# Kernel tuning notes

Hardware: AMD Instinct MI355X
Metric: run time of the kernel (lower is better)

Reference implementation:

```python
import jax, jax.numpy as jnp
import numpy as np

N_NODES = 10000
N_EDGES = 320000
FIN = 2
HID = 64
OUT = 16
B = 4
T = 12


def _gcn_norm(src, dst, w, n):
    # add self loops (fill value 1.0, improved=False), then symmetric normalization
    loop = jnp.arange(n, dtype=src.dtype)
    src = jnp.concatenate([src, loop])
    dst = jnp.concatenate([dst, loop])
    w = jnp.concatenate([w, jnp.ones((n,), w.dtype)])
    deg = jax.ops.segment_sum(w, dst, num_segments=n)
    dinv = jnp.where(deg > 0, 1.0 / jnp.sqrt(deg), 0.0)
    return src, dst, dinv[src] * w * dinv[dst]


def _gcn_conv(x_nbf, src, dst, norm, W, b, n):
    # x_nbf: [N,B,F] ; GCNConv: (x W) aggregated with normalized weights, + bias
    xw = jnp.einsum('nbf,fh->nbh', x_nbf, W)          # [N,B,H]
    msgs = xw[src] * norm[:, None, None]               # [E',B,H]
    return jax.ops.segment_sum(msgs, dst, num_segments=n) + b


def setup_inputs() -> dict:
    key = jax.random.key(0)
    ks = jax.random.split(key, 20)
    x = jax.random.normal(ks[0], (B, N_NODES, FIN, T), jnp.float32)
    edge_index = jax.random.randint(ks[1], (2, N_EDGES), 0, N_NODES, jnp.int64 if jax.config.jax_enable_x64 else jnp.int32)
    edge_weight = jax.random.uniform(ks[2], (N_EDGES,), jnp.float32)
    s = 0.1
    p = {
        'Wz': s * jax.random.normal(ks[3], (FIN, HID), jnp.float32),
        'bz': jnp.zeros((HID,), jnp.float32),
        'Wr': s * jax.random.normal(ks[4], (FIN, HID), jnp.float32),
        'br': jnp.zeros((HID,), jnp.float32),
        'Wh': s * jax.random.normal(ks[5], (FIN, HID), jnp.float32),
        'bh': jnp.zeros((HID,), jnp.float32),
        'Lz_w': s * jax.random.normal(ks[6], (2 * HID, HID), jnp.float32),
        'Lz_b': jnp.zeros((HID,), jnp.float32),
        'Lr_w': s * jax.random.normal(ks[7], (2 * HID, HID), jnp.float32),
        'Lr_b': jnp.zeros((HID,), jnp.float32),
        'Lh_w': s * jax.random.normal(ks[8], (2 * HID, HID), jnp.float32),
        'Lh_b': jnp.zeros((HID,), jnp.float32),
        'lin_w': s * jax.random.normal(ks[9], (HID, OUT), jnp.float32),
        'lin_b': jnp.zeros((OUT,), jnp.float32),
    }
    return dict(x=x, edge_index=edge_index, edge_weight=edge_weight, **p)


def reference(x, edge_index, edge_weight, Wz, bz, Wr, br, Wh, bh,
              Lz_w, Lz_b, Lr_w, Lr_b, Lh_w, Lh_b, lin_w, lin_b):
    Bd, N, Fin, Td = x.shape
    src, dst, norm = _gcn_norm(edge_index[0], edge_index[1], edge_weight, N)
    H0 = jnp.zeros((N, Bd, Wz.shape[1]), x.dtype)
    xs = jnp.transpose(x, (3, 1, 0, 2))  # [T,N,B,Fin]

    def step(H, xt):
        cz = _gcn_conv(xt, src, dst, norm, Wz, bz, N)
        Z = jax.nn.sigmoid(jnp.concatenate([cz, H], -1) @ Lz_w + Lz_b)
        cr = _gcn_conv(xt, src, dst, norm, Wr, br, N)
        R = jax.nn.sigmoid(jnp.concatenate([cr, H], -1) @ Lr_w + Lr_b)
        ch = _gcn_conv(xt, src, dst, norm, Wh, bh, N)
        H_tilde = jnp.tanh(jnp.concatenate([ch, H * R], -1) @ Lh_w + Lh_b)
        Hn = Z * H + (1.0 - Z) * H_tilde
        out_t = jax.nn.relu(Hn) @ lin_w + lin_b  # [N,B,OUT]
        return Hn, out_t

    _, outs = jax.lax.scan(step, H0, xs)        # [T,N,B,OUT]
    return jnp.transpose(outs, (2, 0, 1, 3))     # [B,T,N,OUT]
```

## Files before the change

### kernel.cpp

```cpp
#include <hip/hip_runtime.h>
#include <cstdint>
#include <cstddef>

#define NN      10000
#define NE      320000
#define FINF    2
#define HIDN    64
#define OUTN    16
#define BBATCH  4
#define TSTEPS  12
#define NBROWS  (NN * BBATCH)
#define XTN     (TSTEPS * NN * BBATCH * FINF)
#define CAP     96

typedef _Float16 v8h __attribute__((ext_vector_type(8)));
typedef _Float16 v2h __attribute__((ext_vector_type(2)));
typedef float    v4f __attribute__((ext_vector_type(4)));

extern "C" __global__ void setup_kernel(const float* __restrict__ x,
                             const int* __restrict__ src, const int* __restrict__ dst,
                             const float* __restrict__ ew,
                             int* __restrict__ cnt, float* __restrict__ degf,
                             int2* __restrict__ bucket, _Float16* __restrict__ xAll,
                             const float* __restrict__ Wz, const float* __restrict__ bz,
                             const float* __restrict__ Wr, const float* __restrict__ br,
                             const float* __restrict__ Wh, const float* __restrict__ bh,
                             const float* __restrict__ Lz, const float* __restrict__ Lz_b,
                             const float* __restrict__ Lr, const float* __restrict__ Lr_b,
                             const float* __restrict__ Lh, const float* __restrict__ Lh_b,
                             const float* __restrict__ linw, const float* __restrict__ linb,
                             float* __restrict__ PP) {
    int idx = blockIdx.x * 256 + threadIdx.x;
    if (idx < NN) {
        const int n = idx;
        v8h* xo = (v8h*)(xAll + (size_t)n * 96);
        v8h vv[TSTEPS];
        #pragma unroll
        for (int b = 0; b < BBATCH; ++b) {
            const v4f* xp4 = (const v4f*)(x + ((size_t)b * NN + n) * 24);
            v4f c0 = xp4[0], c1 = xp4[1], c2 = xp4[2];
            v4f c3 = xp4[3], c4 = xp4[4], c5 = xp4[5];
            float f0[TSTEPS] = {c0.x, c0.y, c0.z, c0.w, c1.x, c1.y, c1.z, c1.w,
                                c2.x, c2.y, c2.z, c2.w};
            float f1[TSTEPS] = {c3.x, c3.y, c3.z, c3.w, c4.x, c4.y, c4.z, c4.w,
                                c5.x, c5.y, c5.z, c5.w};
            #pragma unroll
            for (int t = 0; t < TSTEPS; ++t) {
                vv[t][b * 2]     = (_Float16)f0[t];
                vv[t][b * 2 + 1] = (_Float16)f1[t];
            }
        }
        #pragma unroll
        for (int t = 0; t < TSTEPS; ++t) xo[t] = vv[t];
    }
    if (idx < NE) {
        int d = dst[idx];
        int s = src[idx];
        float w = ew[idx];
        int p = atomicAdd(&cnt[d], 1);
        if (p < CAP) {
            int2 rec;
            rec.x = s;
            rec.y = __float_as_int(w);
            bucket[d * CAP + p] = rec;
        }
        atomicAdd(&degf[d], w);
    }
    if (idx < 13904) {
        const float* Lg[3]    = {Lz, Lr, Lh};
        const float* Lbias[3] = {Lz_b, Lr_b, Lh_b};
        const float* Wg[3]    = {Wz, Wr, Wh};
        const float* bg[3]    = {bz, br, bh};
        int i = idx;
        if (i < 12288) {
            int g = i >> 12, rr = (i >> 6) & 63, j = i & 63;
            PP[i] = Lg[g][(64 + rr) * 64 + j];
        } else if (i < 12672) {
            int i2 = i - 12288;
            int g = i2 >> 7, f = (i2 >> 6) & 1, j = i2 & 63;
            float s = 0.f;
            for (int k = 0; k < 64; ++k) s = fmaf(Wg[g][f * 64 + k], Lg[g][k * 64 + j], s);
            PP[i] = s;
        } else if (i < 12864) {
            int i3 = i - 12672;
            int g = i3 >> 6, j = i3 & 63;
            float s = Lbias[g][j];
            for (int k = 0; k < 64; ++k) s = fmaf(bg[g][k], Lg[g][k * 64 + j], s);
            PP[i] = s;
        } else if (i < 13888) {
            PP[i] = linw[i - 12864];
        } else {
            PP[i] = linb[i - 13888];
        }
    }
}

__device__ __forceinline__ float fsigmoid(float x) {
    return __builtin_amdgcn_rcpf(1.0f + __builtin_amdgcn_exp2f(-1.442695041f * x));
}

extern "C" __global__ __launch_bounds__(256, 3)
void fused_kernel(const _Float16* __restrict__ xAll, const int2* __restrict__ bucket,
                  const int* __restrict__ cnt, const float* __restrict__ degf,
                  const float* __restrict__ PP, float* __restrict__ out) {
    __shared__ _Float16 WTH[64 * 72 + 32];
    __shared__ _Float16 WIZR[2 * 64 * 8 + 32];
    __shared__ _Float16 Hm[4][16 * 72];
    __shared__ float    aggL[16 * 96];
    __shared__ int      s_src[16 * CAP];
    __shared__ float    s_c[16 * CAP];
    __shared__ int      s_cnt[16];
    const int tid = threadIdx.x;
    const int w   = tid >> 6;
    const int l   = tid & 63;
    const int m   = l & 15;
    const int q   = l >> 4;
    const int n0  = blockIdx.x * 16 + w * 4 + q;

    {
        const int nl = tid >> 4;
        const int u  = tid & 15;
        const int ng = blockIdx.x * 16 + nl;
        const int c  = min(cnt[ng], CAP);
        if (u == 0) s_cnt[nl] = c;
        const float dn = rsqrtf(1.0f + degf[ng]);
        for (int i = u; i < c; i += 16) {
            int2 rec = bucket[ng * CAP + i];
            int s = rec.x;
            s_src[nl * CAP + i] = s;
            s_c[nl * CAP + i]   = __int_as_float(rec.y) * dn * rsqrtf(1.0f + degf[s]);
        }
    }

    for (int i = tid; i < 4096; i += 256) {
        int k = i >> 6, n = i & 63;
        WTH[n * 72 + k] = (_Float16)PP[8192 + i];
    }
    for (int i = tid; i < 64 * 8; i += 256) {
        int n = i >> 3, kk = i & 7;
        float v = 0.f;
        if (kk == 0)      v = PP[12288 + 2 * 128 + n];
        else if (kk == 1) v = PP[12288 + 2 * 128 + 64 + n];
        else if (kk == 2) v = PP[12672 + 2 * 64 + n];
        WTH[n * 72 + 64 + kk] = (_Float16)v;
    }
    for (int i = tid; i < 32; i += 256) WTH[64 * 72 + i] = (_Float16)0.f;
    for (int i = tid; i < 2 * 64 * 8; i += 256) {
        int g = i >> 9, rem = i & 511, n = rem >> 3, kk = rem & 7;
        float v = 0.f;
        if (kk == 0)      v = PP[12288 + g * 128 + n];
        else if (kk == 1) v = PP[12288 + g * 128 + 64 + n];
        else if (kk == 2) v = PP[12672 + g * 64 + n];
        WIZR[(g * 64 + n) * 8 + kk] = (_Float16)v;
    }
    for (int i = tid; i < 32; i += 256) WIZR[1024 + i] = (_Float16)0.f;

    __syncthreads();

    {
        const int nl = tid >> 4;
        const int u  = tid & 15;
        const int ng = blockIdx.x * 16 + nl;
        const int c  = s_cnt[nl];
        const float dn = rsqrtf(1.0f + degf[ng]);
        const v2h* x2 = (const v2h*)xAll;
        float acc[6];
        {
            v2h a = x2[(size_t)ng * 48 + u * 3];
            v2h b = x2[(size_t)ng * 48 + u * 3 + 1];
            v2h e = x2[(size_t)ng * 48 + u * 3 + 2];
            float c0 = dn * dn;
            acc[0] = c0 * (float)a.x; acc[1] = c0 * (float)a.y;
            acc[2] = c0 * (float)b.x; acc[3] = c0 * (float)b.y;
            acc[4] = c0 * (float)e.x; acc[5] = c0 * (float)e.y;
        }
        for (int i = 0; i < c; ++i) {
            int s    = s_src[nl * CAP + i];
            float cc = s_c[nl * CAP + i];
            v2h a = x2[(size_t)s * 48 + u * 3];
            v2h b = x2[(size_t)s * 48 + u * 3 + 1];
            v2h e = x2[(size_t)s * 48 + u * 3 + 2];
            acc[0] = fmaf(cc, (float)a.x, acc[0]);
            acc[1] = fmaf(cc, (float)a.y, acc[1]);
            acc[2] = fmaf(cc, (float)b.x, acc[2]);
            acc[3] = fmaf(cc, (float)b.y, acc[3]);
            acc[4] = fmaf(cc, (float)e.x, acc[4]);
            acc[5] = fmaf(cc, (float)e.y, acc[5]);
        }
        #pragma unroll
        for (int jj = 0; jj < 6; ++jj) aggL[nl * 96 + u * 6 + jj] = acc[jj];
    }

    v8h BZ[4][2], BR[4][2];
    #pragma unroll
    for (int nt = 0; nt < 4; ++nt) {
        #pragma unroll
        for (int c = 0; c < 2; ++c) {
            #pragma unroll
            for (int i = 0; i < 8; ++i) {
                int k = c * 32 + q * 8 + i;
                BZ[nt][c][i] = (_Float16)PP[k * 64 + nt * 16 + m];
                BR[nt][c][i] = (_Float16)PP[4096 + k * 64 + nt * 16 + m];
            }
        }
    }
    v8h linB0, linB1;
    #pragma unroll
    for (int i = 0; i < 8; ++i) {
        linB0[i] = (_Float16)PP[12864 + (q * 8 + i) * 16 + m];
        linB1[i] = (_Float16)PP[12864 + (32 + q * 8 + i) * 16 + m];
    }
    const float linbv = PP[13888 + m];

    __syncthreads();

    _Float16* __restrict__ Hw = &Hm[w][0];
    const int wsw = (q & 2) << 3;
    const _Float16* __restrict__ Ard = Hw + m * 72 + ((q ^ ((m >> 2) & 2)) * 8);
    const int aggBase = (w * 4 + (m >> 2)) * 96 + (m & 3) * 2;

    float Hold[4][4];
    #pragma unroll
    for (int nt = 0; nt < 4; ++nt)
        #pragma unroll
        for (int r = 0; r < 4; ++r) Hold[nt][r] = 0.f;
    v8h aH0{}, aH1{};

    const v4f zeroc = {0.f, 0.f, 0.f, 0.f};
    float* __restrict__ op = out + (size_t)n0 * 16 + m;

    for (int t = 0; t < TSTEPS; ++t) {
        v8h aI{};
        if (q == 0) {
            const float2 av = *(const float2*)&aggL[aggBase + t * 8];
            aI[0] = (_Float16)av.x;
            aI[1] = (_Float16)av.y;
            aI[2] = (_Float16)1.0f;
        }

        v4f accZ[4], accR[4];
        #pragma unroll
        for (int nt = 0; nt < 4; ++nt) {
            const v8h bIz = *(const v8h*)&WIZR[(0 * 64 + nt * 16 + m) * 8 + q * 8];
            const v8h bIr = *(const v8h*)&WIZR[(1 * 64 + nt * 16 + m) * 8 + q * 8];
            accZ[nt] = __builtin_amdgcn_mfma_f32_16x16x32_f16(aI,  bIz,       zeroc,    0, 0, 0);
            accZ[nt] = __builtin_amdgcn_mfma_f32_16x16x32_f16(aH0, BZ[nt][0], accZ[nt], 0, 0, 0);
            accZ[nt] = __builtin_amdgcn_mfma_f32_16x16x32_f16(aH1, BZ[nt][1], accZ[nt], 0, 0, 0);
            accR[nt] = __builtin_amdgcn_mfma_f32_16x16x32_f16(aI,  bIr,       zeroc,    0, 0, 0);
            accR[nt] = __builtin_amdgcn_mfma_f32_16x16x32_f16(aH0, BR[nt][0], accR[nt], 0, 0, 0);
            accR[nt] = __builtin_amdgcn_mfma_f32_16x16x32_f16(aH1, BR[nt][1], accR[nt], 0, 0, 0);
        }

        float Z[4][4];
        #pragma unroll
        for (int nt = 0; nt < 4; ++nt) {
            #pragma unroll
            for (int r = 0; r < 4; ++r) {
                Z[nt][r] = fsigmoid(accZ[nt][r]);
                float hr = Hold[nt][r] * fsigmoid(accR[nt][r]);
                Hw[(q * 4 + r) * 72 + ((nt * 16 + m) ^ wsw)] = (_Float16)hr;
            }
        }
        __threadfence_block();
        const v8h aP0 = *(const v8h*)Ard;
        const v8h aP1 = *(const v8h*)(Ard + 32);

        v4f accH[4];
        #pragma unroll
        for (int nt = 0; nt < 4; ++nt) {
            const _Float16* bh = &WTH[(nt * 16 + m) * 72 + q * 8];
            accH[nt] = __builtin_amdgcn_mfma_f32_16x16x32_f16(aI,  *(const v8h*)(bh + 64), zeroc,    0, 0, 0);
            accH[nt] = __builtin_amdgcn_mfma_f32_16x16x32_f16(aP0, *(const v8h*)bh,        accH[nt], 0, 0, 0);
            accH[nt] = __builtin_amdgcn_mfma_f32_16x16x32_f16(aP1, *(const v8h*)(bh + 32), accH[nt], 0, 0, 0);
        }

        #pragma unroll
        for (int nt = 0; nt < 4; ++nt) {
            #pragma unroll
            for (int r = 0; r < 4; ++r) {
                float ht = fmaf(2.0f, fsigmoid(2.0f * accH[nt][r]), -1.0f);
                float hn = Z[nt][r] * Hold[nt][r] + (1.f - Z[nt][r]) * ht;
                Hold[nt][r] = hn;
                Hw[(q * 4 + r) * 72 + ((nt * 16 + m) ^ wsw)] = (_Float16)hn;
            }
        }
        __threadfence_block();
        aH0 = *(const v8h*)Ard;
        aH1 = *(const v8h*)(Ard + 32);

        const v8h zz{};
        v8h r0 = __builtin_elementwise_max(aH0, zz);
        v8h r1 = __builtin_elementwise_max(aH1, zz);
        v4f accO = {linbv, linbv, linbv, linbv};
        accO = __builtin_amdgcn_mfma_f32_16x16x32_f16(r0, linB0, accO, 0, 0, 0);
        accO = __builtin_amdgcn_mfma_f32_16x16x32_f16(r1, linB1, accO, 0, 0, 0);
        #pragma unroll
        for (int r = 0; r < 4; ++r)
            op[(size_t)r * (TSTEPS * NN * 16)] = accO[r];
        op += NN * 16;
    }
}


extern "C" void kernel_launch(void* const* d_in, const int* in_sizes, int n_in,
                              void* d_out, int out_size, void* d_ws, size_t ws_size,
                              hipStream_t stream) {
    const float* x   = (const float*)d_in[0];
    const int*   ei  = (const int*)d_in[1];
    const float* ew  = (const float*)d_in[2];
    const float* Wz  = (const float*)d_in[3];
    const float* bz  = (const float*)d_in[4];
    const float* Wr  = (const float*)d_in[5];
    const float* br  = (const float*)d_in[6];
    const float* Wh  = (const float*)d_in[7];
    const float* bh  = (const float*)d_in[8];
    const float* Lz  = (const float*)d_in[9];
    const float* Lz_b= (const float*)d_in[10];
    const float* Lr  = (const float*)d_in[11];
    const float* Lr_b= (const float*)d_in[12];
    const float* Lh  = (const float*)d_in[13];
    const float* Lh_b= (const float*)d_in[14];
    const float* lw  = (const float*)d_in[15];
    const float* lb  = (const float*)d_in[16];
    float* out = (float*)d_out;

    char* ws = (char*)d_ws;
    size_t off = 0;
    auto alloc = [&](size_t bytes) -> char* {
        char* p = ws + off;
        off += (bytes + 15) & ~(size_t)15;
        return p;
    };
    _Float16* xAll = (_Float16*)alloc((size_t)XTN * 2);
    float* PP      = (float*)alloc(13904 * 4);
    int2*  bucket  = (int2*) alloc((size_t)NN * CAP * 8);
    int*   cnt     = (int*)  alloc(NN * 4);
    float* degf    = (float*)alloc(NN * 4);

    const int* srcp = ei;
    const int* dstp = ei + NE;

    hipMemsetAsync(cnt, 0, 2 * NN * sizeof(int), stream);
    setup_kernel<<<(NE + 255) / 256, 256, 0, stream>>>(x, srcp, dstp, ew, cnt, degf,
                                                       bucket, xAll,
                                                       Wz, bz, Wr, br, Wh, bh,
                                                       Lz, Lz_b, Lr, Lr_b, Lh, Lh_b,
                                                       lw, lb, PP);
    fused_kernel<<<NN / 16, 256, 0, stream>>>(xAll, bucket, cnt, degf, PP, out);
}
```

Measured before the change: 193.8 us.

## Merge setup and fused kernels into one persistent kernel with grid barrier

Combines the bucketing/setup kernel and the main recurrent kernel into a single launch, with a global atomic-counter grid barrier between the two phases, which removes one kernel launch and the gap between them. Edge processing becomes a grid-stride loop over 625 blocks. The design depends on all 625 blocks being co-resident (3 blocks per CU is requested on 256 CUs), otherwise the barrier deadlocks. Spinning on the barrier and the smaller grid used for the edge phase can also add latency.

```diff
diff --git a/kernel.cpp b/kernel.cpp
--- a/kernel.cpp
+++ b/kernel.cpp
@@ -12,27 +12,46 @@
 #define NBROWS  (NN * BBATCH)
 #define XTN     (TSTEPS * NN * BBATCH * FINF)
 #define CAP     96
+#define NBLK    (NN / 16)
+#define GT      (NBLK * 256)
 
 typedef _Float16 v8h __attribute__((ext_vector_type(8)));
 typedef _Float16 v2h __attribute__((ext_vector_type(2)));
 typedef float    v4f __attribute__((ext_vector_type(4)));
 
-extern "C" __global__ void setup_kernel(const float* __restrict__ x,
-                             const int* __restrict__ src, const int* __restrict__ dst,
-                             const float* __restrict__ ew,
-                             int* __restrict__ cnt, float* __restrict__ degf,
-                             int2* __restrict__ bucket, _Float16* __restrict__ xAll,
-                             const float* __restrict__ Wz, const float* __restrict__ bz,
-                             const float* __restrict__ Wr, const float* __restrict__ br,
-                             const float* __restrict__ Wh, const float* __restrict__ bh,
-                             const float* __restrict__ Lz, const float* __restrict__ Lz_b,
-                             const float* __restrict__ Lr, const float* __restrict__ Lr_b,
-                             const float* __restrict__ Lh, const float* __restrict__ Lh_b,
-                             const float* __restrict__ linw, const float* __restrict__ linb,
-                             float* __restrict__ PP) {
-    int idx = blockIdx.x * 256 + threadIdx.x;
-    if (idx < NN) {
-        const int n = idx;
+__device__ __forceinline__ float fsigmoid(float x) {
+    return __builtin_amdgcn_rcpf(1.0f + __builtin_amdgcn_exp2f(-1.442695041f * x));
+}
+
+extern "C" __global__ __launch_bounds__(256, 3)
+void mega_kernel(const float* __restrict__ x,
+                 const int* __restrict__ src, const int* __restrict__ dst,
+                 const float* __restrict__ ew,
+                 int* __restrict__ cnt, float* __restrict__ degf,
+                 int2* __restrict__ bucket, _Float16* __restrict__ xAll,
+                 const float* __restrict__ Wz, const float* __restrict__ bz,
+                 const float* __restrict__ Wr, const float* __restrict__ br,
+                 const float* __restrict__ Wh, const float* __restrict__ bh,
+                 const float* __restrict__ Lz, const float* __restrict__ Lz_b,
+                 const float* __restrict__ Lr, const float* __restrict__ Lr_b,
+                 const float* __restrict__ Lh, const float* __restrict__ Lh_b,
+                 const float* __restrict__ linw, const float* __restrict__ linb,
+                 float* __restrict__ PP, int* __restrict__ bar,
+                 float* __restrict__ out) {
+    __shared__ _Float16 WTH[64 * 72 + 32];
+    __shared__ _Float16 WIZR[2 * 64 * 8 + 32];
+    __shared__ _Float16 Hm[4][16 * 72];
+    __shared__ float    aggL[16 * 96];
+    __shared__ int      s_src[16 * CAP];
+    __shared__ float    s_c[16 * CAP];
+    __shared__ int      s_cnt[16];
+
+    const int tid  = threadIdx.x;
+    const int bid  = blockIdx.x;
+    const int gtid = bid * 256 + tid;
+
+    if (gtid < NN) {
+        const int n = gtid;
         v8h* xo = (v8h*)(xAll + (size_t)n * 96);
         v8h vv[TSTEPS];
         #pragma unroll
@@ -53,25 +72,26 @@
         #pragma unroll
         for (int t = 0; t < TSTEPS; ++t) xo[t] = vv[t];
     }
-    if (idx < NE) {
-        int d = dst[idx];
-        int s = src[idx];
-        float w = ew[idx];
+    #pragma unroll
+    for (int e = gtid; e < NE; e += GT) {
+        int d = dst[e];
+        int s = src[e];
+        float wv = ew[e];
         int p = atomicAdd(&cnt[d], 1);
         if (p < CAP) {
             int2 rec;
             rec.x = s;
-            rec.y = __float_as_int(w);
+            rec.y = __float_as_int(wv);
             bucket[d * CAP + p] = rec;
         }
-        atomicAdd(&degf[d], w);
-    }
-    if (idx < 13904) {
+        atomicAdd(&degf[d], wv);
+    }
+    if (gtid < 13904) {
         const float* Lg[3]    = {Lz, Lr, Lh};
         const float* Lbias[3] = {Lz_b, Lr_b, Lh_b};
         const float* Wg[3]    = {Wz, Wr, Wh};
         const float* bg[3]    = {bz, br, bh};
-        int i = idx;
+        int i = gtid;
         if (i < 12288) {
             int g = i >> 12, rr = (i >> 6) & 63, j = i & 63;
             PP[i] = Lg[g][(64 + rr) * 64 + j];
@@ -93,34 +113,27 @@
             PP[i] = linb[i - 13888];
         }
     }
-}
-
-__device__ __forceinline__ float fsigmoid(float x) {
-    return __builtin_amdgcn_rcpf(1.0f + __builtin_amdgcn_exp2f(-1.442695041f * x));
-}
-
-extern "C" __global__ __launch_bounds__(256, 3)
-void fused_kernel(const _Float16* __restrict__ xAll, const int2* __restrict__ bucket,
-                  const int* __restrict__ cnt, const float* __restrict__ degf,
-                  const float* __restrict__ PP, float* __restrict__ out) {
-    __shared__ _Float16 WTH[64 * 72 + 32];
-    __shared__ _Float16 WIZR[2 * 64 * 8 + 32];
-    __shared__ _Float16 Hm[4][16 * 72];
-    __shared__ float    aggL[16 * 96];
-    __shared__ int      s_src[16 * CAP];
-    __shared__ float    s_c[16 * CAP];
-    __shared__ int      s_cnt[16];
-    const int tid = threadIdx.x;
+
+    __syncthreads();
+    if (tid == 0) {
+        __threadfence();
+        __hip_atomic_fetch_add(bar, 1, __ATOMIC_ACQ_REL, __HIP_MEMORY_SCOPE_AGENT);
+        while (__hip_atomic_load(bar, __ATOMIC_ACQUIRE, __HIP_MEMORY_SCOPE_AGENT) < NBLK) {
+            __builtin_amdgcn_s_sleep(8);
+        }
+    }
+    __syncthreads();
+
     const int w   = tid >> 6;
     const int l   = tid & 63;
     const int m   = l & 15;
     const int q   = l >> 4;
-    const int n0  = blockIdx.x * 16 + w * 4 + q;
+    const int n0  = bid * 16 + w * 4 + q;
 
     {
         const int nl = tid >> 4;
         const int u  = tid & 15;
-        const int ng = blockIdx.x * 16 + nl;
+        const int ng = bid * 16 + nl;
         const int c  = min(cnt[ng], CAP);
         if (u == 0) s_cnt[nl] = c;
         const float dn = rsqrtf(1.0f + degf[ng]);
@@ -160,7 +173,7 @@
     {
         const int nl = tid >> 4;
         const int u  = tid & 15;
-        const int ng = blockIdx.x * 16 + nl;
+        const int ng = bid * 16 + nl;
         const int c  = s_cnt[nl];
         const float dn = rsqrtf(1.0f + degf[ng]);
         const v2h* x2 = (const v2h*)xAll;
@@ -336,15 +349,15 @@
     int2*  bucket  = (int2*) alloc((size_t)NN * CAP * 8);
     int*   cnt     = (int*)  alloc(NN * 4);
     float* degf    = (float*)alloc(NN * 4);
+    int*   bar     = (int*)  alloc(16);
 
     const int* srcp = ei;
     const int* dstp = ei + NE;
 
-    hipMemsetAsync(cnt, 0, 2 * NN * sizeof(int), stream);
-    setup_kernel<<<(NE + 255) / 256, 256, 0, stream>>>(x, srcp, dstp, ew, cnt, degf,
-                                                       bucket, xAll,
-                                                       Wz, bz, Wr, br, Wh, bh,
-                                                       Lz, Lz_b, Lr, Lr_b, Lh, Lh_b,
-                                                       lw, lb, PP);
-    fused_kernel<<<NN / 16, 256, 0, stream>>>(xAll, bucket, cnt, degf, PP, out);
+    hipMemsetAsync(cnt, 0, 2 * NN * sizeof(int) + 16, stream);
+    mega_kernel<<<NBLK, 256, 0, stream>>>(x, srcp, dstp, ew, cnt, degf,
+                                          bucket, xAll,
+                                          Wz, bz, Wr, br, Wh, bh,
+                                          Lz, Lz_b, Lr, Lr_b, Lh, Lh_b,
+                                          lw, lb, PP, bar, out);
 }
```

Result: slower. 301.1 us (+55.4%).

## Compute degree from buckets and fold source normalization into packed inputs

Applied to the files above, without the earlier changes.

Drops the per-edge float atomicAdd for degree. Degree is now summed per node from the bucket records in a new prep kernel, which also writes dinv and pre-scales the packed fp16 inputs by the source node's dinv. The fused kernel then needs no per-edge degf gather or rsqrt, and applies the destination dinv once after aggregation. This costs an extra kernel launch and a serial per-node scan of its bucket. The degree also misses edges that overflow the bucket capacity, and fp16 rounding of pre-scaled values changes slightly.

```diff
diff --git a/kernel.cpp b/kernel.cpp
--- a/kernel.cpp
+++ b/kernel.cpp
@@ -17,11 +17,14 @@
 typedef _Float16 v2h __attribute__((ext_vector_type(2)));
 typedef float    v4f __attribute__((ext_vector_type(4)));
 
-extern "C" __global__ void setup_kernel(const float* __restrict__ x,
-                             const int* __restrict__ src, const int* __restrict__ dst,
+__device__ __forceinline__ float fsigmoid(float x) {
+    return __builtin_amdgcn_rcpf(1.0f + __builtin_amdgcn_exp2f(-1.442695041f * x));
+}
+
+extern "C" __global__ void scatter_kernel(const int* __restrict__ src,
+                             const int* __restrict__ dst,
                              const float* __restrict__ ew,
-                             int* __restrict__ cnt, float* __restrict__ degf,
-                             int2* __restrict__ bucket, _Float16* __restrict__ xAll,
+                             int* __restrict__ cnt, int2* __restrict__ bucket,
                              const float* __restrict__ Wz, const float* __restrict__ bz,
                              const float* __restrict__ Wr, const float* __restrict__ br,
                              const float* __restrict__ Wh, const float* __restrict__ bh,
@@ -31,28 +34,6 @@
                              const float* __restrict__ linw, const float* __restrict__ linb,
                              float* __restrict__ PP) {
     int idx = blockIdx.x * 256 + threadIdx.x;
-    if (idx < NN) {
-        const int n = idx;
-        v8h* xo = (v8h*)(xAll + (size_t)n * 96);
-        v8h vv[TSTEPS];
-        #pragma unroll
-        for (int b = 0; b < BBATCH; ++b) {
-            const v4f* xp4 = (const v4f*)(x + ((size_t)b * NN + n) * 24);
-            v4f c0 = xp4[0], c1 = xp4[1], c2 = xp4[2];
-            v4f c3 = xp4[3], c4 = xp4[4], c5 = xp4[5];
-            float f0[TSTEPS] = {c0.x, c0.y, c0.z, c0.w, c1.x, c1.y, c1.z, c1.w,
-                                c2.x, c2.y, c2.z, c2.w};
-            float f1[TSTEPS] = {c3.x, c3.y, c3.z, c3.w, c4.x, c4.y, c4.z, c4.w,
-                                c5.x, c5.y, c5.z, c5.w};
-            #pragma unroll
-            for (int t = 0; t < TSTEPS; ++t) {
-                vv[t][b * 2]     = (_Float16)f0[t];
-                vv[t][b * 2 + 1] = (_Float16)f1[t];
-            }
-        }
-        #pragma unroll
-        for (int t = 0; t < TSTEPS; ++t) xo[t] = vv[t];
-    }
     if (idx < NE) {
         int d = dst[idx];
         int s = src[idx];
@@ -64,7 +45,6 @@
             rec.y = __float_as_int(w);
             bucket[d * CAP + p] = rec;
         }
-        atomicAdd(&degf[d], w);
     }
     if (idx < 13904) {
         const float* Lg[3]    = {Lz, Lr, Lh};
@@ -95,13 +75,44 @@
     }
 }
 
-__device__ __forceinline__ float fsigmoid(float x) {
-    return __builtin_amdgcn_rcpf(1.0f + __builtin_amdgcn_exp2f(-1.442695041f * x));
+extern "C" __global__ void prep_kernel(const float* __restrict__ x,
+                                       const int* __restrict__ cnt,
+                                       const int2* __restrict__ bucket,
+                                       float* __restrict__ dinv,
+                                       _Float16* __restrict__ xAll) {
+    int n = blockIdx.x * 256 + threadIdx.x;
+    if (n >= NN) return;
+    const int c = min(cnt[n], CAP);
+    float deg = 0.f;
+    const int2* bp = bucket + (size_t)n * CAP;
+    for (int i = 0; i < c; ++i) deg += __int_as_float(bp[i].y);
+    const float dv = rsqrtf(1.0f + deg);
+    dinv[n] = dv;
+
+    v8h* xo = (v8h*)(xAll + (size_t)n * 96);
+    v8h vv[TSTEPS];
+    #pragma unroll
+    for (int b = 0; b < BBATCH; ++b) {
+        const v4f* xp4 = (const v4f*)(x + ((size_t)b * NN + n) * 24);
+        v4f c0 = xp4[0], c1 = xp4[1], c2 = xp4[2];
+        v4f c3 = xp4[3], c4 = xp4[4], c5 = xp4[5];
+        float f0[TSTEPS] = {c0.x, c0.y, c0.z, c0.w, c1.x, c1.y, c1.z, c1.w,
+                            c2.x, c2.y, c2.z, c2.w};
+        float f1[TSTEPS] = {c3.x, c3.y, c3.z, c3.w, c4.x, c4.y, c4.z, c4.w,
+                            c5.x, c5.y, c5.z, c5.w};
+        #pragma unroll
+        for (int t = 0; t < TSTEPS; ++t) {
+            vv[t][b * 2]     = (_Float16)(f0[t] * dv);
+            vv[t][b * 2 + 1] = (_Float16)(f1[t] * dv);
+        }
+    }
+    #pragma unroll
+    for (int t = 0; t < TSTEPS; ++t) xo[t] = vv[t];
 }
 
 extern "C" __global__ __launch_bounds__(256, 3)
 void fused_kernel(const _Float16* __restrict__ xAll, const int2* __restrict__ bucket,
-                  const int* __restrict__ cnt, const float* __restrict__ degf,
+                  const int* __restrict__ cnt, const float* __restrict__ dinv,
                   const float* __restrict__ PP, float* __restrict__ out) {
     __shared__ _Float16 WTH[64 * 72 + 32];
     __shared__ _Float16 WIZR[2 * 64 * 8 + 32];
@@ -123,12 +134,10 @@
         const int ng = blockIdx.x * 16 + nl;
         const int c  = min(cnt[ng], CAP);
         if (u == 0) s_cnt[nl] = c;
-        const float dn = rsqrtf(1.0f + degf[ng]);
         for (int i = u; i < c; i += 16) {
             int2 rec = bucket[ng * CAP + i];
-            int s = rec.x;
-            s_src[nl * CAP + i] = s;
-            s_c[nl * CAP + i]   = __int_as_float(rec.y) * dn * rsqrtf(1.0f + degf[s]);
+            s_src[nl * CAP + i] = rec.x;
+            s_c[nl * CAP + i]   = __int_as_float(rec.y);
         }
     }
 
@@ -162,17 +171,16 @@
         const int u  = tid & 15;
         const int ng = blockIdx.x * 16 + nl;
         const int c  = s_cnt[nl];
-        const float dn = rsqrtf(1.0f + degf[ng]);
+        const float dn = dinv[ng];
         const v2h* x2 = (const v2h*)xAll;
         float acc[6];
         {
             v2h a = x2[(size_t)ng * 48 + u * 3];
             v2h b = x2[(size_t)ng * 48 + u * 3 + 1];
             v2h e = x2[(size_t)ng * 48 + u * 3 + 2];
-            float c0 = dn * dn;
-            acc[0] = c0 * (float)a.x; acc[1] = c0 * (float)a.y;
-            acc[2] = c0 * (float)b.x; acc[3] = c0 * (float)b.y;
-            acc[4] = c0 * (float)e.x; acc[5] = c0 * (float)e.y;
+            acc[0] = (float)a.x; acc[1] = (float)a.y;
+            acc[2] = (float)b.x; acc[3] = (float)b.y;
+            acc[4] = (float)e.x; acc[5] = (float)e.y;
         }
         for (int i = 0; i < c; ++i) {
             int s    = s_src[nl * CAP + i];
@@ -188,7 +196,7 @@
             acc[5] = fmaf(cc, (float)e.y, acc[5]);
         }
         #pragma unroll
-        for (int jj = 0; jj < 6; ++jj) aggL[nl * 96 + u * 6 + jj] = acc[jj];
+        for (int jj = 0; jj < 6; ++jj) aggL[nl * 96 + u * 6 + jj] = acc[jj] * dn;
     }
 
     v8h BZ[4][2], BR[4][2];
@@ -335,16 +343,16 @@
     float* PP      = (float*)alloc(13904 * 4);
     int2*  bucket  = (int2*) alloc((size_t)NN * CAP * 8);
     int*   cnt     = (int*)  alloc(NN * 4);
-    float* degf    = (float*)alloc(NN * 4);
+    float* dinv    = (float*)alloc(NN * 4);
 
     const int* srcp = ei;
     const int* dstp = ei + NE;
 
-    hipMemsetAsync(cnt, 0, 2 * NN * sizeof(int), stream);
-    setup_kernel<<<(NE + 255) / 256, 256, 0, stream>>>(x, srcp, dstp, ew, cnt, degf,
-                                                       bucket, xAll,
-                                                       Wz, bz, Wr, br, Wh, bh,
-                                                       Lz, Lz_b, Lr, Lr_b, Lh, Lh_b,
-                                                       lw, lb, PP);
-    fused_kernel<<<NN / 16, 256, 0, stream>>>(xAll, bucket, cnt, degf, PP, out);
-}
+    hipMemsetAsync(cnt, 0, NN * sizeof(int), stream);
+    scatter_kernel<<<(NE + 255) / 256, 256, 0, stream>>>(srcp, dstp, ew, cnt, bucket,
+                                                         Wz, bz, Wr, br, Wh, bh,
+                                                         Lz, Lz_b, Lr, Lr_b, Lh, Lh_b,
+                                                         lw, lb, PP);
+    prep_kernel<<<(NN + 255) / 256, 256, 0, stream>>>(x, cnt, bucket, dinv, xAll);
+    fused_kernel<<<NN / 16, 256, 0, stream>>>(xAll, bucket, cnt, dinv, PP, out);
+}
```

After: 183.1 us. 5.5% less time.
